# Optimization experiments

Measured on AMD Instinct MI355X. Metric: run time of the kernel, lower is better.

## Reference

```python
import jax, jax.numpy as jnp
import numpy as np

N_NODES = 50000
N_EDGES = 800000
D_IN = 128
D_OUT = 64


def setup_inputs() -> dict:
    key = jax.random.key(0)
    k1, k2, k3, k4 = jax.random.split(key, 4)
    x = jax.random.normal(k1, (N_NODES, D_IN), dtype=jnp.float32)
    W = jax.random.normal(k2, (D_OUT, D_IN), dtype=jnp.float32) * (1.0 / np.sqrt(D_IN))
    b = jnp.zeros((D_OUT,), dtype=jnp.float32)
    row = jax.random.randint(k3, (N_EDGES,), 0, N_NODES, dtype=jnp.int32)
    col = jax.random.randint(k4, (N_EDGES,), 0, N_NODES, dtype=jnp.int32)
    return {"x": x, "W": W, "b": b, "row": row, "col": col}


def reference(x, W, b, row, col):
    # Linear projection: [N, D_in] -> [N, D_out]
    h = x @ W.T + b
    n = x.shape[0]
    # Row-normalized SpMM: out[i] = (1/deg(i)) * sum_{(i,j) in E} h[j]
    msg = h[col]  # gather source features: [E, D_out]
    summed = jax.ops.segment_sum(msg, row, num_segments=n)
    deg = jax.ops.segment_sum(jnp.ones_like(row, dtype=h.dtype), row, num_segments=n)
    out = summed / jnp.maximum(deg, 1.0)[:, None]
    return out
```

## Files before the change

kernel.cpp:

```cpp
#include <hip/hip_runtime.h>
#include <hip/hip_bf16.h>

#define D_IN   128
#define D_OUT  64
#define CAP    32
#define MAX_USHORT_NODES 65536
#define BIN_SHIFT 8
#define MAX_BINS  256
#define BIN_CAP   8192
#define P1_BLOCKS 256
#define P2_THREADS 512

using frag_ab = __attribute__((ext_vector_type(8))) short;
using frag_cd = __attribute__((ext_vector_type(4))) float;

static __device__ __forceinline__ short f2bf(float f) {
    union { float f; unsigned u; } v; v.f = f;
    unsigned r = v.u + 0x7FFFu + ((v.u >> 16) & 1u);
    return (short)(r >> 16);
}
static __device__ __forceinline__ float bflo(unsigned w) {
    union { unsigned u; float f; } v; v.u = w << 16; return v.f;
}
static __device__ __forceinline__ float bfhi(unsigned w) {
    union { unsigned u; float f; } v; v.u = w & 0xFFFF0000u; return v.f;
}
static __device__ __forceinline__ float bf1(unsigned short s) {
    union { unsigned u; float f; } v; v.u = ((unsigned)s) << 16; return v.f;
}

__global__ void prep_kernel(const float* __restrict__ x,
                            const float* __restrict__ W,
                            const float* __restrict__ bvec,
                            unsigned short* __restrict__ h,
                            const int* __restrict__ row,
                            const int* __restrict__ col,
                            unsigned* __restrict__ scratch,
                            int* __restrict__ cursor,
                            int* __restrict__ ovfA_cnt,
                            unsigned* __restrict__ ovfA_list,
                            int ovfA_cap, int n_nodes, int n_edges,
                            int n_bins, int proj_blocks) {
    __shared__ int hist[MAX_BINS];
    __shared__ int base[MAX_BINS];

    if ((int)blockIdx.x >= proj_blocks) {
        const int bid = (int)blockIdx.x - proj_blocks;
        const int per = (n_edges + P1_BLOCKS - 1) / P1_BLOCKS;
        const int e0 = bid * per;
        const int e1 = min(e0 + per, n_edges);

        for (int i = threadIdx.x; i < n_bins; i += 256) hist[i] = 0;
        __syncthreads();
        for (int e = e0 + (int)threadIdx.x; e < e1; e += 256)
            atomicAdd(&hist[row[e] >> BIN_SHIFT], 1);
        __syncthreads();
        for (int i = threadIdx.x; i < n_bins; i += 256) {
            const int hcnt = hist[i];
            base[i] = hcnt > 0 ? atomicAdd(&cursor[i * 16], hcnt) : 0;
            hist[i] = 0;
        }
        __syncthreads();
        for (int e = e0 + (int)threadIdx.x; e < e1; e += 256) {
            const int r = row[e];
            const int c = col[e];
            const int bn = r >> BIN_SHIFT;
            const int loc = atomicAdd(&hist[bn], 1);
            const int off = base[bn] + loc;
            if (off < BIN_CAP) {
                scratch[(size_t)bn * BIN_CAP + off] =
                    (unsigned)(r & 255) | ((unsigned)c << 8);
            } else {
                const int k = atomicAdd(ovfA_cnt, 1);
                if (k < ovfA_cap) ovfA_list[k] = (unsigned)r | ((unsigned)c << 16);
            }
        }
        return;
    }

    const int lane = (int)threadIdx.x & 63;
    const int wid  = (int)((blockIdx.x * 256 + threadIdx.x) >> 6);
    const int nwaves = proj_blocks * 4;
    const int m    = lane & 15;
    const int quad = lane >> 4;

    frag_ab Bf[4][4];
#pragma unroll
    for (int kk = 0; kk < 4; ++kk) {
#pragma unroll
        for (int nt = 0; nt < 4; ++nt) {
            const float* wp = W + (size_t)(nt * 16 + m) * D_IN + kk * 32 + quad * 8;
            const float4 w0 = *(const float4*)wp;
            const float4 w1 = *(const float4*)(wp + 4);
            frag_ab f;
            f[0] = f2bf(w0.x); f[1] = f2bf(w0.y); f[2] = f2bf(w0.z); f[3] = f2bf(w0.w);
            f[4] = f2bf(w1.x); f[5] = f2bf(w1.y); f[6] = f2bf(w1.z); f[7] = f2bf(w1.w);
            Bf[kk][nt] = f;
        }
    }
    float bb[4];
#pragma unroll
    for (int nt = 0; nt < 4; ++nt) bb[nt] = bvec[nt * 16 + m];

    const int ntiles = (n_nodes + 15) / 16;
    for (int tile = wid; tile < ntiles; tile += nwaves) {
        const int node_base = tile * 16;
        int arow = node_base + m;
        if (arow > n_nodes - 1) arow = n_nodes - 1;

        float4 xv[8];
        const float* xr = x + (size_t)arow * D_IN + quad * 8;
#pragma unroll
        for (int kk = 0; kk < 4; ++kk) {
            xv[2 * kk]     = *(const float4*)(xr + kk * 32);
            xv[2 * kk + 1] = *(const float4*)(xr + kk * 32 + 4);
        }

        frag_cd acc[4];
#pragma unroll
        for (int nt = 0; nt < 4; ++nt) {
            acc[nt][0] = bb[nt]; acc[nt][1] = bb[nt];
            acc[nt][2] = bb[nt]; acc[nt][3] = bb[nt];
        }
#pragma unroll
        for (int kk = 0; kk < 4; ++kk) {
            const float4 x0 = xv[2 * kk], x1 = xv[2 * kk + 1];
            frag_ab A;
            A[0] = f2bf(x0.x); A[1] = f2bf(x0.y); A[2] = f2bf(x0.z); A[3] = f2bf(x0.w);
            A[4] = f2bf(x1.x); A[5] = f2bf(x1.y); A[6] = f2bf(x1.z); A[7] = f2bf(x1.w);
#pragma unroll
            for (int nt = 0; nt < 4; ++nt)
                acc[nt] = __builtin_amdgcn_mfma_f32_16x16x32_bf16(A, Bf[kk][nt],
                                                                  acc[nt], 0, 0, 0);
        }
#pragma unroll
        for (int nt = 0; nt < 4; ++nt) {
#pragma unroll
            for (int r = 0; r < 4; ++r) {
                const int node = node_base + quad * 4 + r;
                if (node < n_nodes)
                    h[(size_t)node * D_OUT + nt * 16 + m] =
                        (unsigned short)f2bf(acc[nt][r]);
            }
        }
    }
}

__global__ __launch_bounds__(P2_THREADS)
void binpass2_kernel(const unsigned* __restrict__ scratch,
                     const int* __restrict__ cursor,
                     int* __restrict__ deg, unsigned short* __restrict__ bucket,
                     int* __restrict__ ovfB_cnt, unsigned* __restrict__ ovfB_list,
                     int ovfB_cap,
                     const int* __restrict__ ovfA_cnt,
                     const unsigned* __restrict__ ovfA_list, int ovfA_cap,
                     int n_nodes) {
    __shared__ int ldeg[256];
    __shared__ unsigned short lbuck[256 * CAP];
    const int bin = (int)blockIdx.x;
    const int node0 = bin << BIN_SHIFT;
    const int nrows = min(256, n_nodes - node0);
    int cnt = cursor[bin * 16]; if (cnt > BIN_CAP) cnt = BIN_CAP;

    if (bin == 0) {
        int cA = *ovfA_cnt; if (cA > ovfA_cap) cA = ovfA_cap;
        for (int k = threadIdx.x; k < cA; k += P2_THREADS)
            atomicAdd(&deg[ovfA_list[k] & 0xFFFFu], 1);
    }

    for (int i = threadIdx.x; i < 256; i += P2_THREADS) ldeg[i] = 0;
    __syncthreads();
    for (int i = threadIdx.x; i < cnt; i += P2_THREADS) {
        const unsigned rec = scratch[(size_t)bin * BIN_CAP + i];
        const int rl = rec & 255;
        const int c  = (int)(rec >> 8);
        const int s = atomicAdd(&ldeg[rl], 1);
        if (s < CAP) {
            lbuck[(rl << 5) + s] = (unsigned short)c;
        } else {
            const int k = atomicAdd(ovfB_cnt, 1);
            if (k < ovfB_cap)
                ovfB_list[k] = (unsigned)(node0 + rl) | ((unsigned)c << 16);
        }
    }
    __syncthreads();
    for (int i = threadIdx.x; i < nrows; i += P2_THREADS)
        atomicAdd(&deg[node0 + i], ldeg[i]);
    uint4* dst = (uint4*)(bucket + (size_t)node0 * CAP);
    const uint4* src = (const uint4*)lbuck;
    const int nu4 = nrows * (CAP / 8);
    for (int i = threadIdx.x; i < nu4; i += P2_THREADS) dst[i] = src[i];
}

__global__ void gather_kernel(const uint2* __restrict__ h64,
                              const unsigned short* __restrict__ h16,
                              const int* __restrict__ deg,
                              const unsigned short* __restrict__ bucket,
                              const int* __restrict__ ovf_cnts,
                              const unsigned* __restrict__ ovfA_list,
                              const unsigned* __restrict__ ovfB_list,
                              int ovf_cap,
                              float4* __restrict__ out4,
                              int n_nodes) {
    const int lane = (int)threadIdx.x & 63;
    const int q = lane >> 4;
    const int j = lane & 15;
    const int wave = (int)((blockIdx.x * blockDim.x + threadIdx.x) >> 6);
    const int nwaves = (int)((gridDim.x * blockDim.x) >> 6);

    int cA = ovf_cnts[0]; if (cA > ovf_cap) cA = ovf_cap;
    int cB = ovf_cnts[1]; if (cB > ovf_cap) cB = ovf_cap;

    int node = wave;
    if (node >= n_nodes) return;
    int d_nxt = deg[node];
    int my_nxt = (int)bucket[(size_t)node * CAP + (lane & (CAP - 1))];

    while (node < n_nodes) {
        const int d = d_nxt;
        const int mycol = my_nxt;
        const int nxt = node + nwaves;
        if (nxt < n_nodes) {
            d_nxt = deg[nxt];
            my_nxt = (int)bucket[(size_t)nxt * CAP + (lane & (CAP - 1))];
        }

        const int dc = d < CAP ? d : CAP;
        const int ngr = (dc + 3) >> 2;
        float a0 = 0.f, a1 = 0.f, a2 = 0.f, a3 = 0.f;
        float b0 = 0.f, b1 = 0.f, b2 = 0.f, b3 = 0.f;
        int g = 0;
        for (; g + 2 <= ngr; g += 2) {
            const int iA = __shfl(mycol, 4 * g + q);
            const int iB = __shfl(mycol, 4 * g + 4 + q);
            uint2 wA = h64[(size_t)iA * 16 + j];
            uint2 wB = h64[(size_t)iB * 16 + j];
            if (4 * g + q >= dc)     { wA.x = 0u; wA.y = 0u; }
            if (4 * g + 4 + q >= dc) { wB.x = 0u; wB.y = 0u; }
            a0 += bflo(wA.x); a1 += bfhi(wA.x); a2 += bflo(wA.y); a3 += bfhi(wA.y);
            b0 += bflo(wB.x); b1 += bfhi(wB.x); b2 += bflo(wB.y); b3 += bfhi(wB.y);
        }
        for (; g < ngr; ++g) {
            const int iA = __shfl(mycol, 4 * g + q);
            uint2 wA = h64[(size_t)iA * 16 + j];
            if (4 * g + q >= dc) { wA.x = 0u; wA.y = 0u; }
            a0 += bflo(wA.x); a1 += bfhi(wA.x); a2 += bflo(wA.y); a3 += bfhi(wA.y);
        }
        a0 += b0; a1 += b1; a2 += b2; a3 += b3;
        a0 += __shfl_xor(a0, 16); a0 += __shfl_xor(a0, 32);
        a1 += __shfl_xor(a1, 16); a1 += __shfl_xor(a1, 32);
        a2 += __shfl_xor(a2, 16); a2 += __shfl_xor(a2, 32);
        a3 += __shfl_xor(a3, 16); a3 += __shfl_xor(a3, 32);
        if (q == 0) {
            if (cA + cB > 0) {
                for (int k = 0; k < cA; ++k) {
                    const unsigned rec = ovfA_list[k];
                    if ((int)(rec & 0xFFFFu) == node) {
                        const int c = (int)(rec >> 16);
                        a0 += bf1(h16[(size_t)c * D_OUT + 4 * j + 0]);
                        a1 += bf1(h16[(size_t)c * D_OUT + 4 * j + 1]);
                        a2 += bf1(h16[(size_t)c * D_OUT + 4 * j + 2]);
                        a3 += bf1(h16[(size_t)c * D_OUT + 4 * j + 3]);
                    }
                }
                for (int k = 0; k < cB; ++k) {
                    const unsigned rec = ovfB_list[k];
                    if ((int)(rec & 0xFFFFu) == node) {
                        const int c = (int)(rec >> 16);
                        a0 += bf1(h16[(size_t)c * D_OUT + 4 * j + 0]);
                        a1 += bf1(h16[(size_t)c * D_OUT + 4 * j + 1]);
                        a2 += bf1(h16[(size_t)c * D_OUT + 4 * j + 2]);
                        a3 += bf1(h16[(size_t)c * D_OUT + 4 * j + 3]);
                    }
                }
            }
            const float inv = 1.0f / fmaxf((float)d, 1.0f);
            float4 o;
            o.x = a0 * inv; o.y = a1 * inv; o.z = a2 * inv; o.w = a3 * inv;
            out4[(size_t)node * (D_OUT / 4) + j] = o;
        }
        node = nxt;
    }
}

__global__ void proj_only_kernel(const float* __restrict__ x,
                                 const float* __restrict__ W,
                                 const float* __restrict__ bvec,
                                 float* __restrict__ h, int n_nodes) {
    const int lane = (int)threadIdx.x & 63;
    const int wave = (int)((blockIdx.x * blockDim.x + threadIdx.x) >> 6);
    const int nwaves = (int)((gridDim.x * blockDim.x) >> 6);
    const float bias = bvec[lane];
    for (int node = wave; node < n_nodes; node += nwaves) {
        const float* xr = &x[(size_t)node * D_IN];
        float acc = bias;
#pragma unroll
        for (int k = 0; k < D_IN; ++k) acc += xr[k] * W[lane * D_IN + k];
        h[(size_t)node * D_OUT + lane] = acc;
    }
}

__global__ void scatter_kernel(const float* __restrict__ h,
                               const int* __restrict__ row,
                               const int* __restrict__ col,
                               float* __restrict__ out,
                               int* __restrict__ deg,
                               long long n_tasks) {
    long long t = (long long)blockIdx.x * blockDim.x + threadIdx.x;
    const long long stride = (long long)gridDim.x * blockDim.x;
    for (; t < n_tasks; t += stride) {
        const int e = (int)(t >> 6);
        const int c = (int)(t & 63);
        atomicAdd(&out[(size_t)row[e] * D_OUT + c], h[(size_t)col[e] * D_OUT + c]);
        if (c == 0) atomicAdd(&deg[row[e]], 1);
    }
}

__global__ void div_kernel(float* __restrict__ out,
                           const int* __restrict__ deg, int n_total) {
    int t = blockIdx.x * blockDim.x + threadIdx.x;
    if (t < n_total) {
        out[t] *= 1.0f / fmaxf((float)deg[t >> 6], 1.0f);
    }
}

extern "C" void kernel_launch(void* const* d_in, const int* in_sizes, int n_in,
                              void* d_out, int out_size, void* d_ws, size_t ws_size,
                              hipStream_t stream) {
    const float* x   = (const float*)d_in[0];
    const float* W   = (const float*)d_in[1];
    const float* b   = (const float*)d_in[2];
    const int*   row = (const int*)d_in[3];
    const int*   col = (const int*)d_in[4];
    float* out = (float*)d_out;

    const int n_nodes = in_sizes[0] / D_IN;
    const int n_edges = in_sizes[3];
    const int n_bins  = (n_nodes + 255) >> BIN_SHIFT;

    char* p = (char*)d_ws;
    unsigned short* h = (unsigned short*)p;
    p += (size_t)n_nodes * D_OUT * sizeof(unsigned short);
    int* deg = (int*)p;            p += (size_t)n_nodes * sizeof(int);
    int* ovf_cnts = (int*)p;       p += 256;
    int* cursor = (int*)p;         p += (size_t)MAX_BINS * 16 * sizeof(int);
    unsigned* ovfA_list = (unsigned*)p;  p += (size_t)n_edges * sizeof(unsigned);
    unsigned* ovfB_list = (unsigned*)p;  p += (size_t)n_edges * sizeof(unsigned);
    unsigned short* bucket = (unsigned short*)p;
    p += (size_t)n_nodes * CAP * sizeof(unsigned short);
    unsigned* scratch = (unsigned*)p;
    p += (size_t)n_bins * BIN_CAP * sizeof(unsigned);
    const size_t needed = (size_t)(p - (char*)d_ws);

    if (ws_size >= needed && n_nodes <= MAX_USHORT_NODES) {
        hipMemsetAsync(deg, 0,
                       (size_t)n_nodes * sizeof(int) + 256 +
                       (size_t)MAX_BINS * 16 * sizeof(int), stream);

        const int ntiles = (n_nodes + 15) / 16;
        const int proj_blocks = (ntiles + 3) / 4;
        prep_kernel<<<proj_blocks + P1_BLOCKS, 256, 0, stream>>>(
            x, W, b, h, row, col, scratch, cursor, &ovf_cnts[0], ovfA_list,
            n_edges, n_nodes, n_edges, n_bins, proj_blocks);

        binpass2_kernel<<<n_bins, P2_THREADS, 0, stream>>>(
            scratch, cursor, deg, bucket, &ovf_cnts[1], ovfB_list, n_edges,
            &ovf_cnts[0], ovfA_list, n_edges, n_nodes);

        const int grid = (n_nodes + 3) / 4;
        gather_kernel<<<grid, 256, 0, stream>>>(
            (const uint2*)h, h, deg, bucket, ovf_cnts, ovfA_list, ovfB_list,
            n_edges, (float4*)out, n_nodes);
    } else {
        float* hf = (float*)d_ws;
        int* degf = (int*)((char*)d_ws + (size_t)n_nodes * D_OUT * sizeof(float));
        hipMemsetAsync(out, 0, (size_t)out_size * sizeof(float), stream);
        hipMemsetAsync(degf, 0, (size_t)n_nodes * sizeof(int), stream);
        proj_only_kernel<<<1024, 256, 0, stream>>>(x, W, b, hf, n_nodes);
        const long long n_tasks = (long long)n_edges * D_OUT;
        scatter_kernel<<<16384, 256, 0, stream>>>(hf, row, col, out, degf, n_tasks);
        const int n_total = n_nodes * D_OUT;
        div_kernel<<<(n_total + 255) / 256, 256, 0, stream>>>(out, degf, n_total);
    }
}
```

Before: 136.6 us.

## Fuse bin pass and gather into one LDS-accumulating kernel per 128-node bin

Replaces the second binning pass, the per-node bucket build and the separate gather kernel with one kernel per 128-node bin. Each block reads that bin's edge records and accumulates gathered bf16 h rows into an LDS float tile with shared-memory atomics, counts degrees locally, then normalises and writes the output. This removes the bucket and degree round-trips through global memory and one kernel launch. In exchange it relies on LDS float atomics with possible same-row contention, launches only about 391 blocks, and each block scans the whole overflow list serially.

```diff
diff --git a/kernel.cpp b/kernel.cpp
--- a/kernel.cpp
+++ b/kernel.cpp
@@ -3,13 +3,12 @@
 
 #define D_IN   128
 #define D_OUT  64
-#define CAP    32
 #define MAX_USHORT_NODES 65536
-#define BIN_SHIFT 8
-#define MAX_BINS  256
-#define BIN_CAP   8192
-#define P1_BLOCKS 256
-#define P2_THREADS 512
+#define BIN_SHIFT 7
+#define BIN_NODES 128
+#define MAX_BINS  512
+#define BIN_CAP   4096
+#define P1_BLOCKS 128
 
 using frag_ab = __attribute__((ext_vector_type(8))) short;
 using frag_cd = __attribute__((ext_vector_type(4))) float;
@@ -18,12 +17,6 @@
     union { float f; unsigned u; } v; v.f = f;
     unsigned r = v.u + 0x7FFFu + ((v.u >> 16) & 1u);
     return (short)(r >> 16);
-}
-static __device__ __forceinline__ float bflo(unsigned w) {
-    union { unsigned u; float f; } v; v.u = w << 16; return v.f;
-}
-static __device__ __forceinline__ float bfhi(unsigned w) {
-    union { unsigned u; float f; } v; v.u = w & 0xFFFF0000u; return v.f;
 }
 static __device__ __forceinline__ float bf1(unsigned short s) {
     union { unsigned u; float f; } v; v.u = ((unsigned)s) << 16; return v.f;
@@ -69,7 +62,7 @@
             const int off = base[bn] + loc;
             if (off < BIN_CAP) {
                 scratch[(size_t)bn * BIN_CAP + off] =
-                    (unsigned)(r & 255) | ((unsigned)c << 8);
+                    (unsigned)(r & (BIN_NODES - 1)) | ((unsigned)c << BIN_SHIFT);
             } else {
                 const int k = atomicAdd(ovfA_cnt, 1);
                 if (k < ovfA_cap) ovfA_list[k] = (unsigned)r | ((unsigned)c << 16);
@@ -146,140 +139,84 @@
     }
 }
 
-__global__ __launch_bounds__(P2_THREADS)
-void binpass2_kernel(const unsigned* __restrict__ scratch,
-                     const int* __restrict__ cursor,
-                     int* __restrict__ deg, unsigned short* __restrict__ bucket,
-                     int* __restrict__ ovfB_cnt, unsigned* __restrict__ ovfB_list,
-                     int ovfB_cap,
-                     const int* __restrict__ ovfA_cnt,
-                     const unsigned* __restrict__ ovfA_list, int ovfA_cap,
-                     int n_nodes) {
-    __shared__ int ldeg[256];
-    __shared__ unsigned short lbuck[256 * CAP];
+__global__ __launch_bounds__(512)
+void gather2_kernel(const unsigned* __restrict__ scratch,
+                    const int* __restrict__ cursor,
+                    const unsigned short* __restrict__ h16,
+                    const int* __restrict__ ovfA_cnt,
+                    const unsigned* __restrict__ ovfA_list, int ovfA_cap,
+                    float4* __restrict__ out4, int n_nodes) {
+    __shared__ float acc[BIN_NODES * D_OUT];
+    __shared__ int ldeg[BIN_NODES];
     const int bin = (int)blockIdx.x;
     const int node0 = bin << BIN_SHIFT;
-    const int nrows = min(256, n_nodes - node0);
+    const int nrows = min(BIN_NODES, n_nodes - node0);
     int cnt = cursor[bin * 16]; if (cnt > BIN_CAP) cnt = BIN_CAP;
 
-    if (bin == 0) {
-        int cA = *ovfA_cnt; if (cA > ovfA_cap) cA = ovfA_cap;
-        for (int k = threadIdx.x; k < cA; k += P2_THREADS)
-            atomicAdd(&deg[ovfA_list[k] & 0xFFFFu], 1);
-    }
-
-    for (int i = threadIdx.x; i < 256; i += P2_THREADS) ldeg[i] = 0;
+    for (int i = threadIdx.x; i < BIN_NODES * D_OUT; i += 512) acc[i] = 0.f;
+    if (threadIdx.x < BIN_NODES) ldeg[threadIdx.x] = 0;
     __syncthreads();
-    for (int i = threadIdx.x; i < cnt; i += P2_THREADS) {
-        const unsigned rec = scratch[(size_t)bin * BIN_CAP + i];
-        const int rl = rec & 255;
-        const int c  = (int)(rec >> 8);
-        const int s = atomicAdd(&ldeg[rl], 1);
-        if (s < CAP) {
-            lbuck[(rl << 5) + s] = (unsigned short)c;
-        } else {
-            const int k = atomicAdd(ovfB_cnt, 1);
-            if (k < ovfB_cap)
-                ovfB_list[k] = (unsigned)(node0 + rl) | ((unsigned)c << 16);
+
+    const int wv = (int)threadIdx.x >> 6;
+    const int lane = (int)threadIdx.x & 63;
+    const unsigned* sbin = scratch + (size_t)bin * BIN_CAP;
+
+    for (int start = wv * 64; start < cnt; start += 512) {
+        const int nrec = min(64, cnt - start);
+        const unsigned myrec = (lane < nrec) ? sbin[start + lane] : 0u;
+        int g = 0;
+        for (; g + 4 <= nrec; g += 4) {
+            const unsigned r0 = __shfl(myrec, g);
+            const unsigned r1 = __shfl(myrec, g + 1);
+            const unsigned r2 = __shfl(myrec, g + 2);
+            const unsigned r3 = __shfl(myrec, g + 3);
+            const float v0 = bf1(h16[(size_t)(r0 >> BIN_SHIFT) * D_OUT + lane]);
+            const float v1 = bf1(h16[(size_t)(r1 >> BIN_SHIFT) * D_OUT + lane]);
+            const float v2 = bf1(h16[(size_t)(r2 >> BIN_SHIFT) * D_OUT + lane]);
+            const float v3 = bf1(h16[(size_t)(r3 >> BIN_SHIFT) * D_OUT + lane]);
+            atomicAdd(&acc[((r0 & (BIN_NODES - 1)) << 6) + lane], v0);
+            atomicAdd(&acc[((r1 & (BIN_NODES - 1)) << 6) + lane], v1);
+            atomicAdd(&acc[((r2 & (BIN_NODES - 1)) << 6) + lane], v2);
+            atomicAdd(&acc[((r3 & (BIN_NODES - 1)) << 6) + lane], v3);
+            if (lane == 0) {
+                atomicAdd(&ldeg[r0 & (BIN_NODES - 1)], 1);
+                atomicAdd(&ldeg[r1 & (BIN_NODES - 1)], 1);
+                atomicAdd(&ldeg[r2 & (BIN_NODES - 1)], 1);
+                atomicAdd(&ldeg[r3 & (BIN_NODES - 1)], 1);
+            }
+        }
+        for (; g < nrec; ++g) {
+            const unsigned r0 = __shfl(myrec, g);
+            const float v0 = bf1(h16[(size_t)(r0 >> BIN_SHIFT) * D_OUT + lane]);
+            atomicAdd(&acc[((r0 & (BIN_NODES - 1)) << 6) + lane], v0);
+            if (lane == 0) atomicAdd(&ldeg[r0 & (BIN_NODES - 1)], 1);
         }
     }
     __syncthreads();
-    for (int i = threadIdx.x; i < nrows; i += P2_THREADS)
-        atomicAdd(&deg[node0 + i], ldeg[i]);
-    uint4* dst = (uint4*)(bucket + (size_t)node0 * CAP);
-    const uint4* src = (const uint4*)lbuck;
-    const int nu4 = nrows * (CAP / 8);
-    for (int i = threadIdx.x; i < nu4; i += P2_THREADS) dst[i] = src[i];
-}
-
-__global__ void gather_kernel(const uint2* __restrict__ h64,
-                              const unsigned short* __restrict__ h16,
-                              const int* __restrict__ deg,
-                              const unsigned short* __restrict__ bucket,
-                              const int* __restrict__ ovf_cnts,
-                              const unsigned* __restrict__ ovfA_list,
-                              const unsigned* __restrict__ ovfB_list,
-                              int ovf_cap,
-                              float4* __restrict__ out4,
-                              int n_nodes) {
-    const int lane = (int)threadIdx.x & 63;
-    const int q = lane >> 4;
-    const int j = lane & 15;
-    const int wave = (int)((blockIdx.x * blockDim.x + threadIdx.x) >> 6);
-    const int nwaves = (int)((gridDim.x * blockDim.x) >> 6);
-
-    int cA = ovf_cnts[0]; if (cA > ovf_cap) cA = ovf_cap;
-    int cB = ovf_cnts[1]; if (cB > ovf_cap) cB = ovf_cap;
-
-    int node = wave;
-    if (node >= n_nodes) return;
-    int d_nxt = deg[node];
-    int my_nxt = (int)bucket[(size_t)node * CAP + (lane & (CAP - 1))];
-
-    while (node < n_nodes) {
-        const int d = d_nxt;
-        const int mycol = my_nxt;
-        const int nxt = node + nwaves;
-        if (nxt < n_nodes) {
-            d_nxt = deg[nxt];
-            my_nxt = (int)bucket[(size_t)nxt * CAP + (lane & (CAP - 1))];
-        }
-
-        const int dc = d < CAP ? d : CAP;
-        const int ngr = (dc + 3) >> 2;
-        float a0 = 0.f, a1 = 0.f, a2 = 0.f, a3 = 0.f;
-        float b0 = 0.f, b1 = 0.f, b2 = 0.f, b3 = 0.f;
-        int g = 0;
-        for (; g + 2 <= ngr; g += 2) {
-            const int iA = __shfl(mycol, 4 * g + q);
-            const int iB = __shfl(mycol, 4 * g + 4 + q);
-            uint2 wA = h64[(size_t)iA * 16 + j];
-            uint2 wB = h64[(size_t)iB * 16 + j];
-            if (4 * g + q >= dc)     { wA.x = 0u; wA.y = 0u; }
-            if (4 * g + 4 + q >= dc) { wB.x = 0u; wB.y = 0u; }
-            a0 += bflo(wA.x); a1 += bfhi(wA.x); a2 += bflo(wA.y); a3 += bfhi(wA.y);
-            b0 += bflo(wB.x); b1 += bfhi(wB.x); b2 += bflo(wB.y); b3 += bfhi(wB.y);
-        }
-        for (; g < ngr; ++g) {
-            const int iA = __shfl(mycol, 4 * g + q);
-            uint2 wA = h64[(size_t)iA * 16 + j];
-            if (4 * g + q >= dc) { wA.x = 0u; wA.y = 0u; }
-            a0 += bflo(wA.x); a1 += bfhi(wA.x); a2 += bflo(wA.y); a3 += bfhi(wA.y);
-        }
-        a0 += b0; a1 += b1; a2 += b2; a3 += b3;
-        a0 += __shfl_xor(a0, 16); a0 += __shfl_xor(a0, 32);
-        a1 += __shfl_xor(a1, 16); a1 += __shfl_xor(a1, 32);
-        a2 += __shfl_xor(a2, 16); a2 += __shfl_xor(a2, 32);
-        a3 += __shfl_xor(a3, 16); a3 += __shfl_xor(a3, 32);
-        if (q == 0) {
-            if (cA + cB > 0) {
-                for (int k = 0; k < cA; ++k) {
-                    const unsigned rec = ovfA_list[k];
-                    if ((int)(rec & 0xFFFFu) == node) {
-                        const int c = (int)(rec >> 16);
-                        a0 += bf1(h16[(size_t)c * D_OUT + 4 * j + 0]);
-                        a1 += bf1(h16[(size_t)c * D_OUT + 4 * j + 1]);
-                        a2 += bf1(h16[(size_t)c * D_OUT + 4 * j + 2]);
-                        a3 += bf1(h16[(size_t)c * D_OUT + 4 * j + 3]);
-                    }
-                }
-                for (int k = 0; k < cB; ++k) {
-                    const unsigned rec = ovfB_list[k];
-                    if ((int)(rec & 0xFFFFu) == node) {
-                        const int c = (int)(rec >> 16);
-                        a0 += bf1(h16[(size_t)c * D_OUT + 4 * j + 0]);
-                        a1 += bf1(h16[(size_t)c * D_OUT + 4 * j + 1]);
-                        a2 += bf1(h16[(size_t)c * D_OUT + 4 * j + 2]);
-                        a3 += bf1(h16[(size_t)c * D_OUT + 4 * j + 3]);
-                    }
-                }
+
+    int cA = *ovfA_cnt; if (cA > ovfA_cap) cA = ovfA_cap;
+    if (cA > 0 && wv == 0) {
+        for (int k = 0; k < cA; ++k) {
+            const unsigned rec = ovfA_list[k];
+            const int r = (int)(rec & 0xFFFFu);
+            if ((r >> BIN_SHIFT) == bin) {
+                const int c = (int)(rec >> 16);
+                atomicAdd(&acc[((r & (BIN_NODES - 1)) << 6) + lane],
+                          bf1(h16[(size_t)c * D_OUT + lane]));
+                if (lane == 0) atomicAdd(&ldeg[r & (BIN_NODES - 1)], 1);
             }
-            const float inv = 1.0f / fmaxf((float)d, 1.0f);
-            float4 o;
-            o.x = a0 * inv; o.y = a1 * inv; o.z = a2 * inv; o.w = a3 * inv;
-            out4[(size_t)node * (D_OUT / 4) + j] = o;
-        }
-        node = nxt;
+        }
+    }
+    __syncthreads();
+
+    for (int i = threadIdx.x; i < nrows * (D_OUT / 4); i += 512) {
+        const int rl = i >> 4;
+        const int j = i & 15;
+        const float inv = 1.0f / fmaxf((float)ldeg[rl], 1.0f);
+        const float* a = &acc[(rl << 6) + 4 * j];
+        float4 o;
+        o.x = a[0] * inv; o.y = a[1] * inv; o.z = a[2] * inv; o.w = a[3] * inv;
+        out4[(size_t)(node0 + rl) * (D_OUT / 4) + j] = o;
     }
 }
 
@@ -336,26 +273,21 @@
 
     const int n_nodes = in_sizes[0] / D_IN;
     const int n_edges = in_sizes[3];
-    const int n_bins  = (n_nodes + 255) >> BIN_SHIFT;
+    const int n_bins  = (n_nodes + BIN_NODES - 1) >> BIN_SHIFT;
 
     char* p = (char*)d_ws;
     unsigned short* h = (unsigned short*)p;
     p += (size_t)n_nodes * D_OUT * sizeof(unsigned short);
-    int* deg = (int*)p;            p += (size_t)n_nodes * sizeof(int);
     int* ovf_cnts = (int*)p;       p += 256;
     int* cursor = (int*)p;         p += (size_t)MAX_BINS * 16 * sizeof(int);
     unsigned* ovfA_list = (unsigned*)p;  p += (size_t)n_edges * sizeof(unsigned);
-    unsigned* ovfB_list = (unsigned*)p;  p += (size_t)n_edges * sizeof(unsigned);
-    unsigned short* bucket = (unsigned short*)p;
-    p += (size_t)n_nodes * CAP * sizeof(unsigned short);
     unsigned* scratch = (unsigned*)p;
     p += (size_t)n_bins * BIN_CAP * sizeof(unsigned);
     const size_t needed = (size_t)(p - (char*)d_ws);
 
     if (ws_size >= needed && n_nodes <= MAX_USHORT_NODES) {
-        hipMemsetAsync(deg, 0,
-                       (size_t)n_nodes * sizeof(int) + 256 +
-                       (size_t)MAX_BINS * 16 * sizeof(int), stream);
+        hipMemsetAsync(ovf_cnts, 0, 256 + (size_t)MAX_BINS * 16 * sizeof(int),
+                       stream);
 
         const int ntiles = (n_nodes + 15) / 16;
         const int proj_blocks = (ntiles + 3) / 4;
@@ -363,14 +295,9 @@
             x, W, b, h, row, col, scratch, cursor, &ovf_cnts[0], ovfA_list,
             n_edges, n_nodes, n_edges, n_bins, proj_blocks);
 
-        binpass2_kernel<<<n_bins, P2_THREADS, 0, stream>>>(
-            scratch, cursor, deg, bucket, &ovf_cnts[1], ovfB_list, n_edges,
-            &ovf_cnts[0], ovfA_list, n_edges, n_nodes);
-
-        const int grid = (n_nodes + 3) / 4;
-        gather_kernel<<<grid, 256, 0, stream>>>(
-            (const uint2*)h, h, deg, bucket, ovf_cnts, ovfA_list, ovfB_list,
-            n_edges, (float4*)out, n_nodes);
+        gather2_kernel<<<n_bins, 512, 0, stream>>>(
+            scratch, cursor, h, &ovf_cnts[0], ovfA_list, n_edges,
+            (float4*)out, n_nodes);
     } else {
         float* hf = (float*)d_ws;
         int* degf = (int*)((char*)d_ws + (size_t)n_nodes * D_OUT * sizeof(float));
```

Measured after the change: 479.8 us. 251% more time.

## Rewrite gather as one wave per node with lane-per-feature unrolled loads

Applied to the files above, without the earlier changes.

Replaces the grid-stride gather, where 16-lane groups shared the edges, with a kernel that maps one wave to one node and one lane to one output feature. Each wave loads its 32-entry bucket row as scalar-uniform words and issues 16 (or 32 when degree exceeds 16) fully unrolled 2-byte loads that are predicated on degree, so all neighbour loads are in flight at once. This drops the cross-lane shuffles and the xor reduction. In exchange each load is narrower (ushort per lane rather than uint2), it always issues 16 loads even for low-degree nodes (masked entries read node 0's row), and the prefetch of the next node's data is gone.

```diff
diff --git a/kernel.cpp b/kernel.cpp
--- a/kernel.cpp
+++ b/kernel.cpp
@@ -18,12 +18,6 @@
     union { float f; unsigned u; } v; v.f = f;
     unsigned r = v.u + 0x7FFFu + ((v.u >> 16) & 1u);
     return (short)(r >> 16);
-}
-static __device__ __forceinline__ float bflo(unsigned w) {
-    union { unsigned u; float f; } v; v.u = w << 16; return v.f;
-}
-static __device__ __forceinline__ float bfhi(unsigned w) {
-    union { unsigned u; float f; } v; v.u = w & 0xFFFF0000u; return v.f;
 }
 static __device__ __forceinline__ float bf1(unsigned short s) {
     union { unsigned u; float f; } v; v.u = ((unsigned)s) << 16; return v.f;
@@ -192,95 +186,63 @@
     for (int i = threadIdx.x; i < nu4; i += P2_THREADS) dst[i] = src[i];
 }
 
-__global__ void gather_kernel(const uint2* __restrict__ h64,
-                              const unsigned short* __restrict__ h16,
-                              const int* __restrict__ deg,
-                              const unsigned short* __restrict__ bucket,
-                              const int* __restrict__ ovf_cnts,
-                              const unsigned* __restrict__ ovfA_list,
-                              const unsigned* __restrict__ ovfB_list,
-                              int ovf_cap,
-                              float4* __restrict__ out4,
-                              int n_nodes) {
+__global__ __launch_bounds__(256)
+void gather3_kernel(const unsigned short* __restrict__ h16,
+                    const int* __restrict__ deg,
+                    const unsigned short* __restrict__ bucket,
+                    const int* __restrict__ ovf_cnts,
+                    const unsigned* __restrict__ ovfA_list,
+                    const unsigned* __restrict__ ovfB_list,
+                    int ovf_cap,
+                    float* __restrict__ out, int n_nodes) {
     const int lane = (int)threadIdx.x & 63;
-    const int q = lane >> 4;
-    const int j = lane & 15;
-    const int wave = (int)((blockIdx.x * blockDim.x + threadIdx.x) >> 6);
-    const int nwaves = (int)((gridDim.x * blockDim.x) >> 6);
+    const int wv = (int)((blockIdx.x * blockDim.x + threadIdx.x) >> 6);
+    if (wv >= n_nodes) return;
+    const int node = __builtin_amdgcn_readfirstlane(wv);
+
+    const int d = deg[node];
+    const int dc = d < CAP ? d : CAP;
+    const unsigned* brow = (const unsigned*)(bucket + (size_t)node * CAP);
+    unsigned rec[CAP / 2];
+#pragma unroll
+    for (int i = 0; i < CAP / 2; ++i) rec[i] = brow[i];
+
+    float acc = 0.f;
+#pragma unroll
+    for (int k = 0; k < 16; ++k) {
+        const unsigned idx = (k & 1) ? (rec[k >> 1] >> 16)
+                                     : (rec[k >> 1] & 0xFFFFu);
+        const unsigned use = (k < dc) ? idx : 0u;
+        const float v = bf1(h16[(size_t)use * D_OUT + lane]);
+        acc += (k < dc) ? v : 0.f;
+    }
+    if (dc > 16) {
+#pragma unroll
+        for (int k = 16; k < 32; ++k) {
+            const unsigned idx = (k & 1) ? (rec[k >> 1] >> 16)
+                                         : (rec[k >> 1] & 0xFFFFu);
+            const unsigned use = (k < dc) ? idx : 0u;
+            const float v = bf1(h16[(size_t)use * D_OUT + lane]);
+            acc += (k < dc) ? v : 0.f;
+        }
+    }
 
     int cA = ovf_cnts[0]; if (cA > ovf_cap) cA = ovf_cap;
     int cB = ovf_cnts[1]; if (cB > ovf_cap) cB = ovf_cap;
-
-    int node = wave;
-    if (node >= n_nodes) return;
-    int d_nxt = deg[node];
-    int my_nxt = (int)bucket[(size_t)node * CAP + (lane & (CAP - 1))];
-
-    while (node < n_nodes) {
-        const int d = d_nxt;
-        const int mycol = my_nxt;
-        const int nxt = node + nwaves;
-        if (nxt < n_nodes) {
-            d_nxt = deg[nxt];
-            my_nxt = (int)bucket[(size_t)nxt * CAP + (lane & (CAP - 1))];
-        }
-
-        const int dc = d < CAP ? d : CAP;
-        const int ngr = (dc + 3) >> 2;
-        float a0 = 0.f, a1 = 0.f, a2 = 0.f, a3 = 0.f;
-        float b0 = 0.f, b1 = 0.f, b2 = 0.f, b3 = 0.f;
-        int g = 0;
-        for (; g + 2 <= ngr; g += 2) {
-            const int iA = __shfl(mycol, 4 * g + q);
-            const int iB = __shfl(mycol, 4 * g + 4 + q);
-            uint2 wA = h64[(size_t)iA * 16 + j];
-            uint2 wB = h64[(size_t)iB * 16 + j];
-            if (4 * g + q >= dc)     { wA.x = 0u; wA.y = 0u; }
-            if (4 * g + 4 + q >= dc) { wB.x = 0u; wB.y = 0u; }
-            a0 += bflo(wA.x); a1 += bfhi(wA.x); a2 += bflo(wA.y); a3 += bfhi(wA.y);
-            b0 += bflo(wB.x); b1 += bfhi(wB.x); b2 += bflo(wB.y); b3 += bfhi(wB.y);
-        }
-        for (; g < ngr; ++g) {
-            const int iA = __shfl(mycol, 4 * g + q);
-            uint2 wA = h64[(size_t)iA * 16 + j];
-            if (4 * g + q >= dc) { wA.x = 0u; wA.y = 0u; }
-            a0 += bflo(wA.x); a1 += bfhi(wA.x); a2 += bflo(wA.y); a3 += bfhi(wA.y);
-        }
-        a0 += b0; a1 += b1; a2 += b2; a3 += b3;
-        a0 += __shfl_xor(a0, 16); a0 += __shfl_xor(a0, 32);
-        a1 += __shfl_xor(a1, 16); a1 += __shfl_xor(a1, 32);
-        a2 += __shfl_xor(a2, 16); a2 += __shfl_xor(a2, 32);
-        a3 += __shfl_xor(a3, 16); a3 += __shfl_xor(a3, 32);
-        if (q == 0) {
-            if (cA + cB > 0) {
-                for (int k = 0; k < cA; ++k) {
-                    const unsigned rec = ovfA_list[k];
-                    if ((int)(rec & 0xFFFFu) == node) {
-                        const int c = (int)(rec >> 16);
-                        a0 += bf1(h16[(size_t)c * D_OUT + 4 * j + 0]);
-                        a1 += bf1(h16[(size_t)c * D_OUT + 4 * j + 1]);
-                        a2 += bf1(h16[(size_t)c * D_OUT + 4 * j + 2]);
-                        a3 += bf1(h16[(size_t)c * D_OUT + 4 * j + 3]);
-                    }
-                }
-                for (int k = 0; k < cB; ++k) {
-                    const unsigned rec = ovfB_list[k];
-                    if ((int)(rec & 0xFFFFu) == node) {
-                        const int c = (int)(rec >> 16);
-                        a0 += bf1(h16[(size_t)c * D_OUT + 4 * j + 0]);
-                        a1 += bf1(h16[(size_t)c * D_OUT + 4 * j + 1]);
-                        a2 += bf1(h16[(size_t)c * D_OUT + 4 * j + 2]);
-                        a3 += bf1(h16[(size_t)c * D_OUT + 4 * j + 3]);
-                    }
-                }
-            }
-            const float inv = 1.0f / fmaxf((float)d, 1.0f);
-            float4 o;
-            o.x = a0 * inv; o.y = a1 * inv; o.z = a2 * inv; o.w = a3 * inv;
-            out4[(size_t)node * (D_OUT / 4) + j] = o;
-        }
-        node = nxt;
-    }
+    if (cA + cB > 0) {
+        for (int k = 0; k < cA; ++k) {
+            const unsigned r2 = ovfA_list[k];
+            if ((int)(r2 & 0xFFFFu) == node)
+                acc += bf1(h16[(size_t)(r2 >> 16) * D_OUT + lane]);
+        }
+        for (int k = 0; k < cB; ++k) {
+            const unsigned r2 = ovfB_list[k];
+            if ((int)(r2 & 0xFFFFu) == node)
+                acc += bf1(h16[(size_t)(r2 >> 16) * D_OUT + lane]);
+        }
+    }
+
+    out[(size_t)node * D_OUT + lane] = acc * (1.0f / fmaxf((float)d, 1.0f));
 }
 
 __global__ void proj_only_kernel(const float* __restrict__ x,
@@ -368,9 +330,9 @@
             &ovf_cnts[0], ovfA_list, n_edges, n_nodes);
 
         const int grid = (n_nodes + 3) / 4;
-        gather_kernel<<<grid, 256, 0, stream>>>(
-            (const uint2*)h, h, deg, bucket, ovf_cnts, ovfA_list, ovfB_list,
-            n_edges, (float4*)out, n_nodes);
+        gather3_kernel<<<grid, 256, 0, stream>>>(
+            h, deg, bucket, ovf_cnts, ovfA_list, ovfB_list, n_edges,
+            out, n_nodes);
     } else {
         float* hf = (float*)d_ws;
         int* degf = (int*)((char*)d_ws + (size_t)n_nodes * D_OUT * sizeof(float));
```

New measurement: 138.5 us. About the same (+1.4%).
